# Optimization experiments

Hardware: AMD Instinct MI355X
Metric: run time of the kernel (lower is better)

The kernel has to match this reference:

```python
import jax, jax.numpy as jnp
import numpy as np

N_NODES = 50000
N_EDGES = 800000
IN_DIM = 100
OUT_DIM = 40
K_HOPS = 3


def setup_inputs() -> dict:
    key = jax.random.key(0)
    k1, k2, k3, k4 = jax.random.split(key, 4)
    feat = jax.random.normal(k1, (N_NODES, IN_DIM), dtype=jnp.float32)
    # fc params (PyTorch Linear default init scale ~ 1/sqrt(in_dim))
    W = jax.random.normal(k2, (OUT_DIM, IN_DIM), dtype=jnp.float32) / np.sqrt(IN_DIM)
    b = jnp.zeros((OUT_DIM,), dtype=jnp.float32)
    src = jax.random.randint(k3, (N_EDGES,), 0, N_NODES, dtype=jnp.int32)
    dst = jax.random.randint(k4, (N_EDGES,), 0, N_NODES, dtype=jnp.int32)
    return {"feat": feat, "W": W, "b": b, "src": src, "dst": dst}


def reference(feat, W, b, src, dst):
    n = feat.shape[0]
    # symmetric degree norm (DGL SGConv uses in-degrees, clamp(min=1))
    deg = jax.ops.segment_sum(jnp.ones_like(dst, dtype=feat.dtype), dst, num_segments=n)
    norm = jnp.maximum(deg, 1.0)[:, None] ** -0.5  # [N,1]
    h = feat
    for _ in range(K_HOPS):
        h = h * norm
        # SpMM: sum over incoming edges (gather src rows, scatter-add to dst)
        h = jax.ops.segment_sum(h[src], dst, num_segments=n)
        h = h * norm
    # user-supplied normalize: per-feature zero mean / unit std (unbiased std)
    h = (h - h.mean(axis=0)) / h.std(axis=0, ddof=1)
    # final linear classifier
    return h @ W.T + b
```

## Files before the change

### kernel.cpp

```cpp
#include <hip/hip_runtime.h>

#define N_NODES 50000
#define N_EDGES 800000
#define IN_DIM 100
#define OUT_DIM 40
#define ROW 50
#define SCAN_B 512
#define NSCAN_BLK ((N_NODES + SCAN_B - 1) / SCAN_B)

typedef unsigned int uint;

__device__ __forceinline__ float bflo(uint u) { return __uint_as_float(u << 16); }
__device__ __forceinline__ float bfhi(uint u) { return __uint_as_float(u & 0xffff0000u); }
__device__ __forceinline__ uint packbf(float a, float b) {
    uint ua = __float_as_uint(a), ub = __float_as_uint(b);
    ua = (ua + 0x7fffu + ((ua >> 16) & 1u)) >> 16;
    ub = (ub + 0x7fffu + ((ub >> 16) & 1u)) >> 16;
    return ua | (ub << 16);
}

__global__ void zero_kernel(int* p, int n) {
    int i = blockIdx.x * blockDim.x + threadIdx.x;
    if (i < n) p[i] = 0;
}

__global__ void zero_pads_kernel(uint* fs, uint* bufA, uint* bufB) {
    int t = threadIdx.x;
    if (t < ROW) {
        fs[(size_t)N_NODES * ROW + t] = 0u;
        bufA[(size_t)N_NODES * ROW + t] = 0u;
        bufB[(size_t)N_NODES * ROW + t] = 0u;
    }
}

__global__ void deg_kernel(const int* __restrict__ dst, int* __restrict__ deg) {
    int e = blockIdx.x * blockDim.x + threadIdx.x;
    if (e < N_EDGES) atomicAdd(&deg[dst[e]], 1);
}

__global__ __launch_bounds__(SCAN_B) void scan1_kernel(const int* __restrict__ deg,
                                                       int* __restrict__ rowptr,
                                                       float* __restrict__ norm,
                                                       float* __restrict__ norm2,
                                                       int* __restrict__ blocksum) {
    int i = blockIdx.x * SCAN_B + threadIdx.x;
    int lane = threadIdx.x & 63, wid = threadIdx.x >> 6;
    int d = (i < N_NODES) ? deg[i] : 0;
    int v = d;
#pragma unroll
    for (int off = 1; off < 64; off <<= 1) {
        int t = __shfl_up(v, off);
        if (lane >= off) v += t;
    }
    __shared__ int wsum[8];
    if (lane == 63) wsum[wid] = v;
    __syncthreads();
    if (threadIdx.x < 8) {
        int w = wsum[threadIdx.x];
#pragma unroll
        for (int off = 1; off < 8; off <<= 1) {
            int t = __shfl_up(w, off);
            if (lane >= off) w += t;
        }
        wsum[threadIdx.x] = w;
    }
    __syncthreads();
    int woff = wid ? wsum[wid - 1] : 0;
    int incl = woff + v;
    if (i < N_NODES) {
        rowptr[i] = incl - d;
        float n1 = 1.0f / sqrtf((float)max(d, 1));
        norm[i] = n1;
        norm2[i] = n1 * n1;
    }
    if (threadIdx.x == SCAN_B - 1) blocksum[blockIdx.x] = incl;
}

__global__ __launch_bounds__(128) void scan2_kernel(const int* __restrict__ blocksum,
                                                    int* __restrict__ blockoff,
                                                    int* __restrict__ rowptr) {
    __shared__ int s[128];
    int t = threadIdx.x;
    int v = (t < NSCAN_BLK) ? blocksum[t] : 0;
    s[t] = v;
    __syncthreads();
    for (int off = 1; off < 128; off <<= 1) {
        int u = (t >= off) ? s[t - off] : 0;
        __syncthreads();
        s[t] += u;
        __syncthreads();
    }
    if (t < NSCAN_BLK) blockoff[t] = s[t] - v;
    if (t == 127) rowptr[N_NODES] = s[127];
}

__global__ __launch_bounds__(SCAN_B) void scan3_kernel(int* __restrict__ rowptr,
                                                       const int* __restrict__ blockoff) {
    int i = blockIdx.x * SCAN_B + threadIdx.x;
    if (i < N_NODES) rowptr[i] += blockoff[blockIdx.x];
}

__global__ void csr_fill_kernel(const int* __restrict__ src, const int* __restrict__ dst,
                                const int* __restrict__ rowptr, int* __restrict__ cursor,
                                int* __restrict__ csr) {
    int e = blockIdx.x * blockDim.x + threadIdx.x;
    if (e < N_EDGES) {
        int d = dst[e];
        int pos = rowptr[d] + atomicAdd(&cursor[d], 1);
        csr[pos] = src[e];
    }
}

__global__ __launch_bounds__(256) void prescale_kernel(const float* __restrict__ feat,
                                                       const float* __restrict__ norm,
                                                       uint* __restrict__ fs) {
    int i = blockIdx.x * 256 + threadIdx.x;
    if (i < N_NODES * ROW) {
        int n = i / ROW;
        const float2 v = ((const float2*)feat)[i];
        float nm = norm[n];
        fs[i] = packbf(v.x * nm, v.y * nm);
    }
}

__global__ __launch_bounds__(64) void spmm_kernel(const uint* __restrict__ H,
                                                  const int* __restrict__ rowptr,
                                                  const int* __restrict__ csr,
                                                  const float* __restrict__ scale,
                                                  uint* __restrict__ out) {
    const int n = blockIdx.x;
    const int l = threadIdx.x;
    const int ll = min(l, ROW - 1);
    const int beg = rowptr[n], end = rowptr[n + 1];
    float ax = 0.f, ay = 0.f;
    for (int j = beg; j < end; j += 8) {
        int s0 = csr[j];
        int s1 = (j + 1 < end) ? csr[j + 1] : N_NODES;
        int s2 = (j + 2 < end) ? csr[j + 2] : N_NODES;
        int s3 = (j + 3 < end) ? csr[j + 3] : N_NODES;
        int s4 = (j + 4 < end) ? csr[j + 4] : N_NODES;
        int s5 = (j + 5 < end) ? csr[j + 5] : N_NODES;
        int s6 = (j + 6 < end) ? csr[j + 6] : N_NODES;
        int s7 = (j + 7 < end) ? csr[j + 7] : N_NODES;
        uint u0 = H[(size_t)s0 * ROW + ll];
        uint u1 = H[(size_t)s1 * ROW + ll];
        uint u2 = H[(size_t)s2 * ROW + ll];
        uint u3 = H[(size_t)s3 * ROW + ll];
        uint u4 = H[(size_t)s4 * ROW + ll];
        uint u5 = H[(size_t)s5 * ROW + ll];
        uint u6 = H[(size_t)s6 * ROW + ll];
        uint u7 = H[(size_t)s7 * ROW + ll];
        ax += bflo(u0); ay += bfhi(u0);
        ax += bflo(u1); ay += bfhi(u1);
        ax += bflo(u2); ay += bfhi(u2);
        ax += bflo(u3); ay += bfhi(u3);
        ax += bflo(u4); ay += bfhi(u4);
        ax += bflo(u5); ay += bfhi(u5);
        ax += bflo(u6); ay += bfhi(u6);
        ax += bflo(u7); ay += bfhi(u7);
    }
    if (l < ROW) {
        float sc = scale[n];
        out[(size_t)n * ROW + l] = packbf(ax * sc, ay * sc);
    }
}

#define CS_BLOCKS 625
#define CS_THREADS 256
__global__ __launch_bounds__(CS_THREADS) void col_stats_kernel(const uint* __restrict__ h,
                                                               float* __restrict__ colsum,
                                                               float* __restrict__ colsq) {
    int gtid = blockIdx.x * CS_THREADS + threadIdx.x;
    const int stride = CS_BLOCKS * CS_THREADS;
    float s0 = 0.f, s1 = 0.f, q0 = 0.f, q1 = 0.f;
    for (int i = gtid; i < N_NODES * ROW; i += stride) {
        uint u = h[i];
        float a = bflo(u), b = bfhi(u);
        s0 += a; s1 += b; q0 += a * a; q1 += b * b;
    }
    __shared__ float ssum[IN_DIM], ssq[IN_DIM];
    if (threadIdx.x < IN_DIM) { ssum[threadIdx.x] = 0.f; ssq[threadIdx.x] = 0.f; }
    __syncthreads();
    int p = gtid % ROW;
    atomicAdd(&ssum[2 * p], s0);
    atomicAdd(&ssum[2 * p + 1], s1);
    atomicAdd(&ssq[2 * p], q0);
    atomicAdd(&ssq[2 * p + 1], q1);
    __syncthreads();
    if (threadIdx.x < IN_DIM) {
        atomicAdd(&colsum[threadIdx.x], ssum[threadIdx.x]);
        atomicAdd(&colsq[threadIdx.x], ssq[threadIdx.x]);
    }
}

__global__ __launch_bounds__(256) void prep_kernel(const float* __restrict__ colsum,
                                                   const float* __restrict__ colsq,
                                                   const float* __restrict__ W,
                                                   const float* __restrict__ b,
                                                   float* __restrict__ Wt,
                                                   float* __restrict__ bp) {
    __shared__ float smean[IN_DIM];
    __shared__ float sinv[IN_DIM];
    int t = threadIdx.x;
    const float Nf = (float)N_NODES;
    if (t < IN_DIM) {
        float m = colsum[t] / Nf;
        float var = (colsq[t] - Nf * m * m) / (Nf - 1.0f);
        var = fmaxf(var, 1e-20f);
        smean[t] = m;
        sinv[t] = 1.0f / sqrtf(var);
    }
    __syncthreads();
    for (int i = t; i < IN_DIM * OUT_DIM; i += 256) {
        int o = i % OUT_DIM, f = i / OUT_DIM;
        Wt[f * OUT_DIM + o] = W[o * IN_DIM + f] * sinv[f];
    }
    if (t < OUT_DIM) {
        float acc = b[t];
        for (int f = 0; f < IN_DIM; ++f)
            acc -= smean[f] * W[t * IN_DIM + f] * sinv[f];
        bp[t] = acc;
    }
}

__global__ __launch_bounds__(256) void final_kernel(const uint* __restrict__ h,
                                                    const float* __restrict__ Wt,
                                                    const float* __restrict__ bp,
                                                    float* __restrict__ out) {
    __shared__ float sW[IN_DIM * OUT_DIM];
    __shared__ float sb[OUT_DIM];
    for (int i = threadIdx.x; i < IN_DIM * OUT_DIM; i += 256) sW[i] = Wt[i];
    if (threadIdx.x < OUT_DIM) sb[threadIdx.x] = bp[threadIdx.x];
    __syncthreads();
    int t = blockIdx.x * 256 + threadIdx.x;
    if (t >= N_NODES * OUT_DIM) return;
    int n = t / OUT_DIM;
    int o = t - n * OUT_DIM;
    const uint* hr = h + (size_t)n * ROW;
    float acc = sb[o];
#pragma unroll 10
    for (int p = 0; p < ROW; ++p) {
        uint u = hr[p];
        acc += bflo(u) * sW[(2 * p) * OUT_DIM + o];
        acc += bfhi(u) * sW[(2 * p + 1) * OUT_DIM + o];
    }
    out[t] = acc;
}

extern "C" void kernel_launch(void* const* d_in, const int* in_sizes, int n_in,
                              void* d_out, int out_size, void* d_ws, size_t ws_size,
                              hipStream_t stream) {
    const float* feat = (const float*)d_in[0];
    const float* W    = (const float*)d_in[1];
    const float* b    = (const float*)d_in[2];
    const int*   src  = (const int*)d_in[3];
    const int*   dst  = (const int*)d_in[4];
    float* out = (float*)d_out;

    char* w = (char*)d_ws;
    int*   deg      = (int*)w;    w += N_NODES * 4;
    int*   cursor   = (int*)w;    w += N_NODES * 4;
    float* colsum   = (float*)w;  w += 128 * 4;
    float* colsq    = (float*)w;  w += 128 * 4;
    int*   rowptr   = (int*)w;    w += 50004 * 4;
    float* norm     = (float*)w;  w += N_NODES * 4;
    float* norm2    = (float*)w;  w += N_NODES * 4;
    int*   blocksum = (int*)w;    w += 128 * 4;
    int*   blockoff = (int*)w;    w += 128 * 4;
    int*   csr      = (int*)w;    w += N_EDGES * 4;
    float* Wt       = (float*)w;  w += IN_DIM * OUT_DIM * 4;
    float* bp       = (float*)w;  w += 64 * 4;
    const size_t HB = ((size_t)(N_NODES + 1) * ROW + 16) * 4;
    uint*  fs       = (uint*)w;   w += HB;
    uint*  bufA     = (uint*)w;   w += HB;
    uint*  bufB     = (uint*)w;   w += HB;

    {
        int nz = N_NODES * 2 + 256;
        zero_kernel<<<(nz + 255) / 256, 256, 0, stream>>>(deg, nz);
        zero_pads_kernel<<<1, 64, 0, stream>>>(fs, bufA, bufB);
    }
    deg_kernel<<<(N_EDGES + 255) / 256, 256, 0, stream>>>(dst, deg);
    scan1_kernel<<<NSCAN_BLK, SCAN_B, 0, stream>>>(deg, rowptr, norm, norm2, blocksum);
    scan2_kernel<<<1, 128, 0, stream>>>(blocksum, blockoff, rowptr);
    scan3_kernel<<<NSCAN_BLK, SCAN_B, 0, stream>>>(rowptr, blockoff);
    csr_fill_kernel<<<(N_EDGES + 255) / 256, 256, 0, stream>>>(src, dst, rowptr, cursor, csr);
    prescale_kernel<<<(N_NODES * ROW + 255) / 256, 256, 0, stream>>>(feat, norm, fs);
    spmm_kernel<<<N_NODES, 64, 0, stream>>>(fs, rowptr, csr, norm2, bufA);
    spmm_kernel<<<N_NODES, 64, 0, stream>>>(bufA, rowptr, csr, norm2, bufB);
    spmm_kernel<<<N_NODES, 64, 0, stream>>>(bufB, rowptr, csr, norm, bufA);
    col_stats_kernel<<<CS_BLOCKS, CS_THREADS, 0, stream>>>(bufA, colsum, colsq);
    prep_kernel<<<1, 256, 0, stream>>>(colsum, colsq, W, b, Wt, bp);
    {
        int total = N_NODES * OUT_DIM;
        final_kernel<<<(total + 255) / 256, 256, 0, stream>>>(bufA, Wt, bp, out);
    }
}
```

Baseline: 305.0 us.

## Merge pad zeroing, reuse degree atomics for CSR, widen SpMM blocks and unroll

Pad zeroing is folded into the zero kernel, which drops one launch. The offsets returned by the degree atomics are stored per edge, so the CSR fill no longer needs a second atomic pass or a cursor array. The SpMM kernel now handles two nodes per 128-thread block and gathers 16 neighbours per iteration instead of 8, exposing more memory-level parallelism. In exchange, the per-edge offset array costs extra workspace and traffic, and the wider unroll raises register use and wastes padded loads on low-degree rows.

```diff
diff --git a/kernel.cpp b/kernel.cpp
--- a/kernel.cpp
+++ b/kernel.cpp
@@ -19,23 +19,20 @@
     return ua | (ub << 16);
 }
 
-__global__ void zero_kernel(int* p, int n) {
+__global__ void zero_kernel(int* p, int n, uint* fs, uint* bufA, uint* bufB) {
     int i = blockIdx.x * blockDim.x + threadIdx.x;
     if (i < n) p[i] = 0;
-}
-
-__global__ void zero_pads_kernel(uint* fs, uint* bufA, uint* bufB) {
-    int t = threadIdx.x;
-    if (t < ROW) {
-        fs[(size_t)N_NODES * ROW + t] = 0u;
-        bufA[(size_t)N_NODES * ROW + t] = 0u;
-        bufB[(size_t)N_NODES * ROW + t] = 0u;
-    }
-}
-
-__global__ void deg_kernel(const int* __restrict__ dst, int* __restrict__ deg) {
+    if (i < ROW) {
+        fs[(size_t)N_NODES * ROW + i] = 0u;
+        bufA[(size_t)N_NODES * ROW + i] = 0u;
+        bufB[(size_t)N_NODES * ROW + i] = 0u;
+    }
+}
+
+__global__ void deg_kernel(const int* __restrict__ dst, int* __restrict__ deg,
+                           int* __restrict__ eoff) {
     int e = blockIdx.x * blockDim.x + threadIdx.x;
-    if (e < N_EDGES) atomicAdd(&deg[dst[e]], 1);
+    if (e < N_EDGES) eoff[e] = atomicAdd(&deg[dst[e]], 1);
 }
 
 __global__ __launch_bounds__(SCAN_B) void scan1_kernel(const int* __restrict__ deg,
@@ -101,14 +98,11 @@
 }
 
 __global__ void csr_fill_kernel(const int* __restrict__ src, const int* __restrict__ dst,
-                                const int* __restrict__ rowptr, int* __restrict__ cursor,
+                                const int* __restrict__ rowptr,
+                                const int* __restrict__ eoff,
                                 int* __restrict__ csr) {
     int e = blockIdx.x * blockDim.x + threadIdx.x;
-    if (e < N_EDGES) {
-        int d = dst[e];
-        int pos = rowptr[d] + atomicAdd(&cursor[d], 1);
-        csr[pos] = src[e];
-    }
+    if (e < N_EDGES) csr[rowptr[dst[e]] + eoff[e]] = src[e];
 }
 
 __global__ __launch_bounds__(256) void prescale_kernel(const float* __restrict__ feat,
@@ -123,41 +117,27 @@
     }
 }
 
-__global__ __launch_bounds__(64) void spmm_kernel(const uint* __restrict__ H,
-                                                  const int* __restrict__ rowptr,
-                                                  const int* __restrict__ csr,
-                                                  const float* __restrict__ scale,
-                                                  uint* __restrict__ out) {
-    const int n = blockIdx.x;
-    const int l = threadIdx.x;
+__global__ __launch_bounds__(128) void spmm_kernel(const uint* __restrict__ H,
+                                                   const int* __restrict__ rowptr,
+                                                   const int* __restrict__ csr,
+                                                   const float* __restrict__ scale,
+                                                   uint* __restrict__ out) {
+    const int n = blockIdx.x * 2 + (threadIdx.x >> 6);
+    const int l = threadIdx.x & 63;
     const int ll = min(l, ROW - 1);
     const int beg = rowptr[n], end = rowptr[n + 1];
     float ax = 0.f, ay = 0.f;
-    for (int j = beg; j < end; j += 8) {
-        int s0 = csr[j];
-        int s1 = (j + 1 < end) ? csr[j + 1] : N_NODES;
-        int s2 = (j + 2 < end) ? csr[j + 2] : N_NODES;
-        int s3 = (j + 3 < end) ? csr[j + 3] : N_NODES;
-        int s4 = (j + 4 < end) ? csr[j + 4] : N_NODES;
-        int s5 = (j + 5 < end) ? csr[j + 5] : N_NODES;
-        int s6 = (j + 6 < end) ? csr[j + 6] : N_NODES;
-        int s7 = (j + 7 < end) ? csr[j + 7] : N_NODES;
-        uint u0 = H[(size_t)s0 * ROW + ll];
-        uint u1 = H[(size_t)s1 * ROW + ll];
-        uint u2 = H[(size_t)s2 * ROW + ll];
-        uint u3 = H[(size_t)s3 * ROW + ll];
-        uint u4 = H[(size_t)s4 * ROW + ll];
-        uint u5 = H[(size_t)s5 * ROW + ll];
-        uint u6 = H[(size_t)s6 * ROW + ll];
-        uint u7 = H[(size_t)s7 * ROW + ll];
-        ax += bflo(u0); ay += bfhi(u0);
-        ax += bflo(u1); ay += bfhi(u1);
-        ax += bflo(u2); ay += bfhi(u2);
-        ax += bflo(u3); ay += bfhi(u3);
-        ax += bflo(u4); ay += bfhi(u4);
-        ax += bflo(u5); ay += bfhi(u5);
-        ax += bflo(u6); ay += bfhi(u6);
-        ax += bflo(u7); ay += bfhi(u7);
+    for (int j = beg; j < end; j += 16) {
+        int s[16];
+#pragma unroll
+        for (int k = 0; k < 16; ++k)
+            s[k] = (j + k < end) ? csr[j + k] : N_NODES;
+        uint u[16];
+#pragma unroll
+        for (int k = 0; k < 16; ++k)
+            u[k] = H[(size_t)s[k] * ROW + ll];
+#pragma unroll
+        for (int k = 0; k < 16; ++k) { ax += bflo(u[k]); ay += bfhi(u[k]); }
     }
     if (l < ROW) {
         float sc = scale[n];
@@ -259,15 +239,15 @@
 
     char* w = (char*)d_ws;
     int*   deg      = (int*)w;    w += N_NODES * 4;
-    int*   cursor   = (int*)w;    w += N_NODES * 4;
     float* colsum   = (float*)w;  w += 128 * 4;
     float* colsq    = (float*)w;  w += 128 * 4;
+    int*   eoff     = (int*)w;    w += N_EDGES * 4;
     int*   rowptr   = (int*)w;    w += 50004 * 4;
     float* norm     = (float*)w;  w += N_NODES * 4;
     float* norm2    = (float*)w;  w += N_NODES * 4;
     int*   blocksum = (int*)w;    w += 128 * 4;
     int*   blockoff = (int*)w;    w += 128 * 4;
-    int*   csr      = (int*)w;    w += N_EDGES * 4;
+    int*   csr      = (int*)w;    w += (N_EDGES + 64) * 4;
     float* Wt       = (float*)w;  w += IN_DIM * OUT_DIM * 4;
     float* bp       = (float*)w;  w += 64 * 4;
     const size_t HB = ((size_t)(N_NODES + 1) * ROW + 16) * 4;
@@ -276,19 +256,18 @@
     uint*  bufB     = (uint*)w;   w += HB;
 
     {
-        int nz = N_NODES * 2 + 256;
-        zero_kernel<<<(nz + 255) / 256, 256, 0, stream>>>(deg, nz);
-        zero_pads_kernel<<<1, 64, 0, stream>>>(fs, bufA, bufB);
-    }
-    deg_kernel<<<(N_EDGES + 255) / 256, 256, 0, stream>>>(dst, deg);
+        int nz = N_NODES + 256;
+        zero_kernel<<<(nz + 255) / 256, 256, 0, stream>>>(deg, nz, fs, bufA, bufB);
+    }
+    deg_kernel<<<(N_EDGES + 255) / 256, 256, 0, stream>>>(dst, deg, eoff);
     scan1_kernel<<<NSCAN_BLK, SCAN_B, 0, stream>>>(deg, rowptr, norm, norm2, blocksum);
     scan2_kernel<<<1, 128, 0, stream>>>(blocksum, blockoff, rowptr);
     scan3_kernel<<<NSCAN_BLK, SCAN_B, 0, stream>>>(rowptr, blockoff);
-    csr_fill_kernel<<<(N_EDGES + 255) / 256, 256, 0, stream>>>(src, dst, rowptr, cursor, csr);
+    csr_fill_kernel<<<(N_EDGES + 255) / 256, 256, 0, stream>>>(src, dst, rowptr, eoff, csr);
     prescale_kernel<<<(N_NODES * ROW + 255) / 256, 256, 0, stream>>>(feat, norm, fs);
-    spmm_kernel<<<N_NODES, 64, 0, stream>>>(fs, rowptr, csr, norm2, bufA);
-    spmm_kernel<<<N_NODES, 64, 0, stream>>>(bufA, rowptr, csr, norm2, bufB);
-    spmm_kernel<<<N_NODES, 64, 0, stream>>>(bufB, rowptr, csr, norm, bufA);
+    spmm_kernel<<<N_NODES / 2, 128, 0, stream>>>(fs, rowptr, csr, norm2, bufA);
+    spmm_kernel<<<N_NODES / 2, 128, 0, stream>>>(bufA, rowptr, csr, norm2, bufB);
+    spmm_kernel<<<N_NODES / 2, 128, 0, stream>>>(bufB, rowptr, csr, norm, bufA);
     col_stats_kernel<<<CS_BLOCKS, CS_THREADS, 0, stream>>>(bufA, colsum, colsq);
     prep_kernel<<<1, 256, 0, stream>>>(colsum, colsq, W, b, Wt, bp);
     {
```

Result: slower. 331.2 us (+8.6%).
